# Optimization experiments

Hardware: AMD Instinct MI355X
Metric: run time of the kernel (lower is better)

## Reference

```python
import jax, jax.numpy as jnp
import numpy as np

B, T, D, H = 4, 2048, 1024, 16
DH = D // H
SCALE = 1.0 / np.sqrt(DH)


def setup_inputs() -> dict:
    key = jax.random.key(0)
    ks = jax.random.split(key, 8)
    s = 1.0 / np.sqrt(D)  # keep projections well-scaled
    return {
        "query": jax.random.normal(ks[0], (B, T, D), jnp.float32),
        "key": jax.random.normal(ks[1], (B, T, D), jnp.float32),
        "value": jax.random.normal(ks[2], (B, T, D), jnp.float32),
        "Wq": jax.random.normal(ks[3], (D, D), jnp.float32) * s,
        "bq": jnp.zeros((D,), jnp.float32),
        "Wk": jax.random.normal(ks[4], (D, D), jnp.float32) * s,
        "bk": jnp.zeros((D,), jnp.float32),
        "Wv": jax.random.normal(ks[5], (D, D), jnp.float32) * s,
        "bv": jnp.zeros((D,), jnp.float32),
        "Wo": jax.random.normal(ks[6], (D, D), jnp.float32) * s,
        "bo": jnp.zeros((D,), jnp.float32),
    }


def reference(query, key, value, Wq, bq, Wk, bk, Wv, bv, Wo, bo):
    # Linear projections (torch Linear: x @ W.T + b; W here stored as [out,in])
    Q = query @ Wq.T + bq            # [B,T,D]
    K = key @ Wk.T + bk
    V = value @ Wv.T + bv
    # split heads -> [B,H,T,DH]
    Q = Q.reshape(B, T, H, DH).transpose(0, 2, 1, 3)
    K = K.reshape(B, T, H, DH).transpose(0, 2, 1, 3)
    V = V.reshape(B, T, H, DH).transpose(0, 2, 1, 3)
    # scaled dot-product attention (chunking in the original is a memory
    # optimization, not a math change; no mask, eval-mode dropout = identity)
    scores = jnp.einsum("bhqd,bhkd->bhqk", Q, K) * SCALE
    attn = jax.nn.softmax(scores, axis=-1)
    out = jnp.einsum("bhqk,bhkd->bhqd", attn, V)  # [B,H,T,DH]
    out = out.transpose(0, 2, 1, 3).reshape(B, T, D)
    return out @ Wo.T + bo
```

## Files before the change

### kernel.cpp

```cpp
#include <hip/hip_runtime.h>
#include <hip/hip_bf16.h>

typedef __bf16 bf16x8 __attribute__((ext_vector_type(8)));
typedef float f32x4 __attribute__((ext_vector_type(4)));
typedef float f32x16 __attribute__((ext_vector_type(16)));
typedef unsigned int uint;
typedef unsigned short u16;

#define DEV static __device__ __forceinline__

DEV u16 f2bf(float x) {
    uint u = __builtin_bit_cast(uint, x);
    u += 0x7FFFu + ((u >> 16) & 1u);
    return (u16)(u >> 16);
}

DEV uint cvtpk(float lo, float hi) {
    uint r;
    asm("v_cvt_pk_bf16_f32 %0, %1, %2" : "=v"(r) : "v"(lo), "v"(hi));
    return r;
}

DEV void plswap(uint& a, uint& b) {
    asm("v_permlane32_swap_b32 %0, %1" : "+v"(a), "+v"(b));
}

DEV float max3f(float a, float b, float c) {
    float d;
    asm("v_max3_f32 %0, %1, %2, %3" : "=v"(d) : "v"(a), "v"(b), "v"(c));
    return d;
}

DEV float fexp2(float x) { return __builtin_amdgcn_exp2f(x); }

DEV void gload16(const void* g, void* l) {
    __builtin_amdgcn_global_load_lds((const __attribute__((address_space(1))) void*)g,
                                     (__attribute__((address_space(3))) void*)l,
                                     16, 0, 0);
}

DEV uint4 xpose8(uint4 vd, int l) {
    uint w0 = vd.x, w1 = vd.y, w2 = vd.z, w3 = vd.w;
    {
        int lam = (l >> 5) & 1;
        uint s0 = lam ? w0 : w2, s1 = lam ? w1 : w3;
        uint t0 = __shfl_xor(s0, 32), t1 = __shfl_xor(s1, 32);
        if (lam) { w0 = t0; w1 = t1; } else { w2 = t0; w3 = t1; }
    }
    {
        int lam = (l >> 4) & 1;
        uint s0 = lam ? w0 : w1, s1 = lam ? w2 : w3;
        uint t0 = __shfl_xor(s0, 16), t1 = __shfl_xor(s1, 16);
        if (lam) { w0 = t0; w2 = t1; } else { w1 = t0; w3 = t1; }
    }
    {
        int lam = (l >> 3) & 1;
        uint sA = lam ? ((w0 & 0xFFFFu) | (w1 << 16)) : ((w0 >> 16) | (w1 & 0xFFFF0000u));
        uint sB = lam ? ((w2 & 0xFFFFu) | (w3 << 16)) : ((w2 >> 16) | (w3 & 0xFFFF0000u));
        uint tA = __shfl_xor(sA, 8), tB = __shfl_xor(sB, 8);
        if (lam) {
            w0 = (w0 & 0xFFFF0000u) | (tA & 0xFFFFu);
            w1 = (w1 & 0xFFFF0000u) | (tA >> 16);
            w2 = (w2 & 0xFFFF0000u) | (tB & 0xFFFFu);
            w3 = (w3 & 0xFFFF0000u) | (tB >> 16);
        } else {
            w0 = (w0 & 0xFFFFu) | (tA << 16);
            w1 = (w1 & 0xFFFFu) | (tA & 0xFFFF0000u);
            w2 = (w2 & 0xFFFFu) | (tB << 16);
            w3 = (w3 & 0xFFFFu) | (tB & 0xFFFF0000u);
        }
    }
    return make_uint4(w0, w1, w2, w3);
}

__global__ __launch_bounds__(256) void k_wconv(const float* __restrict__ w0,
                                               const float* __restrict__ w1,
                                               const float* __restrict__ w2,
                                               const float* __restrict__ w3,
                                               u16* __restrict__ out) {
    const int which = blockIdx.x >> 9;
    const float* in = which == 0 ? w0 : (which == 1 ? w1 : (which == 2 ? w2 : w3));
    const long i = (blockIdx.x & 511) * 256 + threadIdx.x;
    const float4* p = (const float4*)in + i * 2;
    float4 a = p[0], b = p[1];
    uint4 dv;
    dv.x = cvtpk(a.x, a.y); dv.y = cvtpk(a.z, a.w);
    dv.z = cvtpk(b.x, b.y); dv.w = cvtpk(b.z, b.w);
    ((uint4*)(out + ((long)which << 20)))[i] = dv;
}

__global__ __launch_bounds__(256, 2) void k_gemm_qkv(
    const float* __restrict__ Aq, const float* __restrict__ Ak,
    const float* __restrict__ Av, const u16* __restrict__ Bw,
    const float* __restrict__ b0, const float* __restrict__ b1,
    const float* __restrict__ b2, u16* __restrict__ Cb) {
    constexpr int N = 1024, K = 1024;
    __shared__ u16 lA[128 * 64];
    __shared__ u16 lB[128 * 64];
    const int tid = threadIdx.x;
    const int l = tid & 63, w = tid >> 6;
    const int lr = l & 15, lk = l >> 4;
    const int wr = w >> 1, wc = w & 1;
    const int nbn = N >> 7;
    const int cpx = (int)gridDim.x >> 3;
    const int wg = (blockIdx.x & 7) * cpx + (blockIdx.x >> 3);
    const int bm = wg / nbn, bn = wg % nbn;
    const int seg = bm >> 6;
    const float* Aseg = seg == 0 ? Aq : (seg == 1 ? Ak : Av);
    const u16* Bseg = Bw + ((long)seg << 20);
    const float* bias = seg == 0 ? b0 : (seg == 1 ? b1 : b2);
    const int bml = bm & 63;

    const int arow = tid >> 3;
    const int acol = (tid & 7) * 8;
    int adst[4];
    const float* asrc[4];
#pragma unroll
    for (int t = 0; t < 4; ++t) {
        int row = t * 32 + arow;
        adst[t] = row * 128 + ((acol * 2) ^ ((row & 7) << 4));
        asrc[t] = Aseg + (long)(bml * 128 + row) * K + acol;
    }
    long bbase[4];
    int bdst[4];
#pragma unroll
    for (int t = 0; t < 4; ++t) {
        int p = (t * 256 + tid) * 16;
        int row = p >> 7;
        int src = (p & 127) ^ ((row & 7) << 4);
        bdst[t] = p;
        bbase[t] = (long)(bn * 128 + row) * (K * 2) + src;
    }
    const int swz = (lr & 7) << 4;
    int aoff[4][2], boff[4][2];
#pragma unroll
    for (int m = 0; m < 4; ++m)
#pragma unroll
        for (int kc = 0; kc < 2; ++kc) {
            aoff[m][kc] = (wr * 64 + m * 16 + lr) * 128 + ((kc * 64 + lk * 16) ^ swz);
            boff[m][kc] = (wc * 64 + m * 16 + lr) * 128 + ((kc * 64 + lk * 16) ^ swz);
        }

    f32x4 acc[4][4] = {};
    const char* gB = (const char*)Bseg;
    const char* lAb = (const char*)lA;
    const char* lBb = (const char*)lB;
    for (int kt = 0; kt < K / 64; ++kt) {
        __syncthreads();
#pragma unroll
        for (int t = 0; t < 4; ++t)
            gload16(gB + bbase[t] + kt * 128, (char*)lB + bdst[t]);
        float4 f0[4], f1[4];
#pragma unroll
        for (int t = 0; t < 4; ++t) {
            const float* s = asrc[t] + kt * 64;
            f0[t] = *(const float4*)s;
            f1[t] = *(const float4*)(s + 4);
        }
#pragma unroll
        for (int t = 0; t < 4; ++t) {
            uint4 dv;
            dv.x = cvtpk(f0[t].x, f0[t].y);
            dv.y = cvtpk(f0[t].z, f0[t].w);
            dv.z = cvtpk(f1[t].x, f1[t].y);
            dv.w = cvtpk(f1[t].z, f1[t].w);
            *(uint4*)((char*)lA + adst[t]) = dv;
        }
        __syncthreads();
#pragma unroll
        for (int kc = 0; kc < 2; ++kc) {
            bf16x8 av[4], bv[4];
#pragma unroll
            for (int m = 0; m < 4; ++m) av[m] = *(const bf16x8*)(lAb + aoff[m][kc]);
#pragma unroll
            for (int n = 0; n < 4; ++n) bv[n] = *(const bf16x8*)(lBb + boff[n][kc]);
#pragma unroll
            for (int m = 0; m < 4; ++m)
#pragma unroll
                for (int n = 0; n < 4; ++n)
                    acc[m][n] = __builtin_amdgcn_mfma_f32_16x16x32_bf16(av[m], bv[n], acc[m][n], 0, 0, 0);
        }
    }

    const int col0 = bn * 128 + wc * 64;
    float bval[4];
#pragma unroll
    for (int n = 0; n < 4; ++n) bval[n] = bias[col0 + n * 16 + lr];
    const int row0 = bm * 128 + wr * 64;
#pragma unroll
    for (int m = 0; m < 4; ++m)
#pragma unroll
        for (int j = 0; j < 4; ++j) {
            int row = row0 + m * 16 + lk * 4 + j;
#pragma unroll
            for (int n = 0; n < 4; ++n)
                Cb[(long)row * N + col0 + n * 16 + lr] = f2bf(acc[m][n][j] + bval[n]);
        }
}

__global__ __launch_bounds__(256) void k_vtrans(const u16* __restrict__ V,
                                                u16* __restrict__ VT) {
    __shared__ u16 lds[64 * 40];
    const int tid = threadIdx.x;
    const int l = tid & 63, w = tid >> 6;
    const int vr = l >> 3, vdb = l & 7;
    const int bid = blockIdx.x;
    const int bh = bid & 63, tc = bid >> 6;
    const int b = bh >> 4, h = bh & 15;
    const int t0 = tc * 32;

    const u16* src = V + ((long)(b * 2048 + t0 + w * 8 + vr) * 1024 + h * 64 + vdb * 8);
    uint4 vd = *(const uint4*)src;
    uint4 tt = xpose8(vd, l);
    *(uint4*)((char*)lds + (vdb * 8 + vr) * 80 + w * 16) = tt;
    __syncthreads();
    const int ch2 = tid >> 2, part = tid & 3;
    uint4 r = *(const uint4*)((const char*)lds + ch2 * 80 + part * 16);
    *(uint4*)(VT + ((long)(bh * 64 + ch2) * 2048 + t0 + part * 8)) = r;
}

__global__ __launch_bounds__(256, 2) void k_gemm_bt(
    const u16* __restrict__ A, const u16* __restrict__ Bw,
    const float* __restrict__ bias, float* __restrict__ Cf,
    int M, int N, int K) {
    __shared__ u16 lA[128 * 64];
    __shared__ u16 lB[128 * 64];
    const int tid = threadIdx.x;
    const int l = tid & 63, w = tid >> 6;
    const int lr = l & 15, lk = l >> 4;
    const int wr = w >> 1, wc = w & 1;
    const int nbn = N >> 7;
    const int cpx = (int)gridDim.x >> 3;
    const int wg = (blockIdx.x & 7) * cpx + (blockIdx.x >> 3);
    const int bm = wg / nbn, bn = wg % nbn;

    long abase[4], bbase[4];
    int ldst[4];
#pragma unroll
    for (int t = 0; t < 4; ++t) {
        int c = t * 256 + tid;
        int p = c * 16;
        int row = p >> 7;
        int inrow = p & 127;
        int src = inrow ^ ((row & 7) << 4);
        ldst[t] = p;
        abase[t] = (long)(bm * 128 + row) * (K * 2) + src;
        bbase[t] = (long)(bn * 128 + row) * (K * 2) + src;
    }
    const int swz = (lr & 7) << 4;
    int aoff[4][2], boff[4][2];
#pragma unroll
    for (int m = 0; m < 4; ++m)
#pragma unroll
        for (int kc = 0; kc < 2; ++kc) {
            aoff[m][kc] = (wr * 64 + m * 16 + lr) * 128 + ((kc * 64 + lk * 16) ^ swz);
            boff[m][kc] = (wc * 64 + m * 16 + lr) * 128 + ((kc * 64 + lk * 16) ^ swz);
        }

    f32x4 acc[4][4] = {};
    const char* gA = (const char*)A;
    const char* gB = (const char*)Bw;
    const char* lAb = (const char*)lA;
    const char* lBb = (const char*)lB;
    const int nkt = K >> 6;
    for (int kt = 0; kt < nkt; ++kt) {
        __syncthreads();
#pragma unroll
        for (int t = 0; t < 4; ++t)
            gload16(gA + abase[t] + kt * 128, (char*)lA + ldst[t]);
#pragma unroll
        for (int t = 0; t < 4; ++t)
            gload16(gB + bbase[t] + kt * 128, (char*)lB + ldst[t]);
        __syncthreads();
#pragma unroll
        for (int kc = 0; kc < 2; ++kc) {
            bf16x8 av[4], bv[4];
#pragma unroll
            for (int m = 0; m < 4; ++m) av[m] = *(const bf16x8*)(lAb + aoff[m][kc]);
#pragma unroll
            for (int n = 0; n < 4; ++n) bv[n] = *(const bf16x8*)(lBb + boff[n][kc]);
#pragma unroll
            for (int m = 0; m < 4; ++m)
#pragma unroll
                for (int n = 0; n < 4; ++n)
                    acc[m][n] = __builtin_amdgcn_mfma_f32_16x16x32_bf16(av[m], bv[n], acc[m][n], 0, 0, 0);
        }
    }

    const int row0 = bm * 128 + wr * 64;
    const int col0 = bn * 128 + wc * 64;
    float bval[4];
#pragma unroll
    for (int n = 0; n < 4; ++n) bval[n] = bias[col0 + n * 16 + lr];
#pragma unroll
    for (int m = 0; m < 4; ++m)
#pragma unroll
        for (int j = 0; j < 4; ++j) {
            int row = row0 + m * 16 + lk * 4 + j;
#pragma unroll
            for (int n = 0; n < 4; ++n)
                Cf[(long)row * N + col0 + n * 16 + lr] = acc[m][n][j] + bval[n];
        }
}

__global__ __launch_bounds__(512, 4) void k_attn5(
    const u16* __restrict__ Qb, const u16* __restrict__ Kb,
    const u16* __restrict__ VTb, u16* __restrict__ Ob) {
    constexpr int T = 2048, D = 1024;
    constexpr int NT = T / 64;
    __shared__ u16 sK[2][4096];
    __shared__ u16 sV[2][4096];
    const int tid = threadIdx.x;
    const int l = tid & 63, w = tid >> 6;
    const int hi = l >> 5;
    const int q32 = l & 31;
    const int hi16 = hi * 16;
    const int kswz = (q32 & 7) << 4;
    const int bid = blockIdx.x;
    const int bh = (bid & 7) * 8 + ((bid >> 3) & 7);
    const int qt = bid >> 6;
    const int b = bh >> 4, h = bh & 15;

    const char* Qg = (const char*)(Qb + (long)b * T * D + h * 64);
    const char* Kg = (const char*)(Kb + (long)b * T * D + h * 64);
    const char* VTg = (const char*)(VTb + (long)bh * 64 * 2048);
    const int q0 = qt * 256 + w * 32;

    bf16x8 qf[4];
#pragma unroll
    for (int c = 0; c < 4; ++c)
        qf[c] = *(const bf16x8*)(Qg + (long)(q0 + q32) * 2048 + c * 32 + hi16);

    const int srow = tid >> 3;
    const int ssrc = ((tid & 7) * 16) ^ ((srow & 7) << 4);
    const int sdst = tid * 16;
    const long kbase = (long)srow * 2048 + ssrc;
    const long vbase = (long)srow * 4096 + ssrc;

    union { u16 s[8]; bf16x8 v; } ones_u;
#pragma unroll
    for (int i = 0; i < 8; ++i) ones_u.s[i] = 0x3F80;
    const bf16x8 onesv = ones_u.v;

#define STAGE(kt_, buf_) do {                                                  \
        gload16(Kg + (long)(kt_) * 64 * 2048 + kbase, (char*)sK[buf_] + sdst); \
        gload16(VTg + (kt_) * 128 + vbase, (char*)sV[buf_] + sdst);            \
    } while (0)

    STAGE(0, 0);
    __syncthreads();

    f32x16 o[2] = {};
    f32x16 lacc = {};
    float m = -1e30f;
    const float k1 = 0.18033688f;
    const float THR = 44.3616f;

    for (int kt = 0; kt < NT; ++kt) {
        if (kt + 1 < NT) STAGE(kt + 1, (kt + 1) & 1);

        const char* kbp = (const char*)sK[kt & 1];
        f32x16 st[2] = {};
        __builtin_amdgcn_s_setprio(1);
#pragma unroll
        for (int c = 0; c < 4; ++c) {
            bf16x8 kf = *(const bf16x8*)(kbp + q32 * 128 + ((c * 32 + hi16) ^ kswz));
            st[0] = __builtin_amdgcn_mfma_f32_32x32x16_bf16(kf, qf[c], st[0], 0, 0, 0);
        }
#pragma unroll
        for (int c = 0; c < 4; ++c) {
            bf16x8 kf = *(const bf16x8*)(kbp + (32 + q32) * 128 + ((c * 32 + hi16) ^ kswz));
            st[1] = __builtin_amdgcn_mfma_f32_32x32x16_bf16(kf, qf[c], st[1], 0, 0, 0);
        }
        __builtin_amdgcn_s_setprio(0);

        float t0 = max3f(st[0][0], st[0][1], st[0][2]);
        float t1 = max3f(st[0][3], st[0][4], st[0][5]);
        float t2 = max3f(st[0][6], st[0][7], st[0][8]);
        float t3 = max3f(st[0][9], st[0][10], st[0][11]);
        float t4 = max3f(st[0][12], st[0][13], st[0][14]);
        float t5 = max3f(st[1][0], st[1][1], st[1][2]);
        float t6 = max3f(st[1][3], st[1][4], st[1][5]);
        float t7 = max3f(st[1][6], st[1][7], st[1][8]);
        float t8 = max3f(st[1][9], st[1][10], st[1][11]);
        float t9 = max3f(st[1][12], st[1][13], st[1][14]);
        float u0 = max3f(t0, t1, t2);
        float u1 = max3f(t3, t4, st[0][15]);
        float u2 = max3f(t5, t6, t7);
        float u3 = max3f(t8, t9, st[1][15]);
        float rm = fmaxf(max3f(u0, u1, u2), u3);

        bool defer = __all(rm <= m + THR);
        if (!defer) {
            float rmw = fmaxf(rm, __shfl_xor(rm, 32));
            float mn = fmaxf(m, rmw);
            float aq = fexp2((m - mn) * k1);
            m = mn;
#pragma unroll
            for (int r = 0; r < 16; ++r) {
                int src = (r & 3) + 8 * (r >> 2) + 4 * hi;
                float ar = __shfl(aq, src);
                o[0][r] *= ar;
                o[1][r] *= ar;
                lacc[r] *= ar;
            }
        }
        float mk = m * k1;
#pragma unroll
        for (int n = 0; n < 2; ++n)
#pragma unroll
            for (int r = 0; r < 16; ++r)
                st[n][r] = fexp2(fmaf(st[n][r], k1, -mk));

        const char* vbp = (const char*)sV[kt & 1];
        __builtin_amdgcn_s_setprio(1);
#pragma unroll
        for (int c = 0; c < 4; ++c) {
            const int n = c >> 1, rb = (c & 1) * 8;
            uint A0 = cvtpk(st[n][rb + 0], st[n][rb + 1]);
            uint A1 = cvtpk(st[n][rb + 2], st[n][rb + 3]);
            uint B0 = cvtpk(st[n][rb + 4], st[n][rb + 5]);
            uint B1 = cvtpk(st[n][rb + 6], st[n][rb + 7]);
            plswap(A0, B0);
            plswap(A1, B1);
            union { uint u[4]; bf16x8 v; } pa;
            pa.u[0] = A0; pa.u[1] = A1; pa.u[2] = B0; pa.u[3] = B1;
            int cb = c * 32 + hi16;
            bf16x8 v0 = *(const bf16x8*)(vbp + q32 * 128 + (cb ^ kswz));
            bf16x8 v1 = *(const bf16x8*)(vbp + (32 + q32) * 128 + (cb ^ kswz));
            o[0] = __builtin_amdgcn_mfma_f32_32x32x16_bf16(pa.v, v0, o[0], 0, 0, 0);
            o[1] = __builtin_amdgcn_mfma_f32_32x32x16_bf16(pa.v, v1, o[1], 0, 0, 0);
            lacc  = __builtin_amdgcn_mfma_f32_32x32x16_bf16(pa.v, onesv, lacc, 0, 0, 0);
        }
        __builtin_amdgcn_s_setprio(0);
        __syncthreads();
    }
#undef STAGE

#pragma unroll
    for (int r = 0; r < 16; ++r) {
        float inv = 1.f / lacc[r];
        int srcq = (r & 3) + 8 * (r >> 2) + 4 * hi;
        int trow = q0 + srcq;
        char* orow = (char*)Ob + ((long)(b * T + trow) * D + h * 64) * 2;
        *(u16*)(orow + q32 * 2) = f2bf(o[0][r] * inv);
        *(u16*)(orow + (32 + q32) * 2) = f2bf(o[1][r] * inv);
    }
}

extern "C" void kernel_launch(void* const* d_in, const int* in_sizes, int n_in,
                              void* d_out, int out_size, void* d_ws, size_t ws_size,
                              hipStream_t stream) {
    const float* q  = (const float*)d_in[0];
    const float* k  = (const float*)d_in[1];
    const float* v  = (const float*)d_in[2];
    const float* Wq = (const float*)d_in[3];
    const float* bq = (const float*)d_in[4];
    const float* Wk = (const float*)d_in[5];
    const float* bk = (const float*)d_in[6];
    const float* Wv = (const float*)d_in[7];
    const float* bv = (const float*)d_in[8];
    const float* Wo = (const float*)d_in[9];
    const float* bo = (const float*)d_in[10];

    const long MT = 8192L * 1024;
    const long WT = 1024L * 1024;
    u16* ws   = (u16*)d_ws;
    u16* wall = ws;
    u16* qbf  = wall + 4 * WT;
    u16* kbf  = qbf + MT;
    u16* vbf  = kbf + MT;
    u16* vtb  = vbf + MT;
    u16* abf  = vtb + MT;

    k_wconv<<<dim3(2048), dim3(256), 0, stream>>>(Wq, Wk, Wv, Wo, wall);

    k_gemm_qkv<<<dim3(1536), dim3(256), 0, stream>>>(q, k, v, wall,
                                                     bq, bk, bv, qbf);

    k_vtrans<<<dim3(4096), dim3(256), 0, stream>>>(vbf, vtb);

    k_attn5<<<dim3(512), dim3(512), 0, stream>>>(qbf, kbf, vtb, abf);

    k_gemm_bt<<<dim3(512), dim3(256), 0, stream>>>(abf, wall + 3 * WT, bo,
                                                   (float*)d_out, 8192, 1024, 1024);
}
```

Baseline: 192.9 us.

## Double-buffer LDS tiles in QKV GEMM to overlap global loads with MFMA

New measurement: 201.8 us. +4.6%, slower.

```diff
diff --git a/kernel.cpp b/kernel.cpp
--- a/kernel.cpp
+++ b/kernel.cpp
@@ -95,8 +95,8 @@
     const float* __restrict__ b0, const float* __restrict__ b1,
     const float* __restrict__ b2, u16* __restrict__ Cb) {
     constexpr int N = 1024, K = 1024;
-    __shared__ u16 lA[128 * 64];
-    __shared__ u16 lB[128 * 64];
+    __shared__ u16 lA[2][8192];
+    __shared__ u16 lB[2][8192];
     const int tid = threadIdx.x;
     const int l = tid & 63, w = tid >> 6;
     const int lr = l & 15, lk = l >> 4;
@@ -143,30 +143,46 @@
 
     f32x4 acc[4][4] = {};
     const char* gB = (const char*)Bseg;
-    const char* lAb = (const char*)lA;
-    const char* lBb = (const char*)lB;
+    float4 f0[4], f1[4];
+
+#define LOADA(kt_) do {                                                        \
+        _Pragma("unroll")                                                      \
+        for (int t = 0; t < 4; ++t) {                                          \
+            const float* s = asrc[t] + (kt_) * 64;                             \
+            f0[t] = *(const float4*)s;                                         \
+            f1[t] = *(const float4*)(s + 4);                                   \
+        }                                                                      \
+    } while (0)
+#define WRITEA(buf_) do {                                                      \
+        _Pragma("unroll")                                                      \
+        for (int t = 0; t < 4; ++t) {                                          \
+            uint4 dv;                                                          \
+            dv.x = cvtpk(f0[t].x, f0[t].y);                                    \
+            dv.y = cvtpk(f0[t].z, f0[t].w);                                    \
+            dv.z = cvtpk(f1[t].x, f1[t].y);                                    \
+            dv.w = cvtpk(f1[t].z, f1[t].w);                                    \
+            *(uint4*)((char*)lA[buf_] + adst[t]) = dv;                         \
+        }                                                                      \
+    } while (0)
+#define LOADB(kt_, buf_) do {                                                  \
+        _Pragma("unroll")                                                      \
+        for (int t = 0; t < 4; ++t)                                            \
+            gload16(gB + bbase[t] + (kt_) * 128, (char*)lB[buf_] + bdst[t]);   \
+    } while (0)
+
+    LOADA(0);
+    LOADB(0, 0);
+    WRITEA(0);
+    __syncthreads();
+
     for (int kt = 0; kt < K / 64; ++kt) {
-        __syncthreads();
-#pragma unroll
-        for (int t = 0; t < 4; ++t)
-            gload16(gB + bbase[t] + kt * 128, (char*)lB + bdst[t]);
-        float4 f0[4], f1[4];
-#pragma unroll
-        for (int t = 0; t < 4; ++t) {
-            const float* s = asrc[t] + kt * 64;
-            f0[t] = *(const float4*)s;
-            f1[t] = *(const float4*)(s + 4);
-        }
-#pragma unroll
-        for (int t = 0; t < 4; ++t) {
-            uint4 dv;
-            dv.x = cvtpk(f0[t].x, f0[t].y);
-            dv.y = cvtpk(f0[t].z, f0[t].w);
-            dv.z = cvtpk(f1[t].x, f1[t].y);
-            dv.w = cvtpk(f1[t].z, f1[t].w);
-            *(uint4*)((char*)lA + adst[t]) = dv;
-        }
-        __syncthreads();
+        const int cur = kt & 1;
+        if (kt + 1 < K / 64) {
+            LOADB(kt + 1, cur ^ 1);
+            LOADA(kt + 1);
+        }
+        const char* lAb = (const char*)lA[cur];
+        const char* lBb = (const char*)lB[cur];
 #pragma unroll
         for (int kc = 0; kc < 2; ++kc) {
             bf16x8 av[4], bv[4];
@@ -180,7 +196,13 @@
                 for (int n = 0; n < 4; ++n)
                     acc[m][n] = __builtin_amdgcn_mfma_f32_16x16x32_bf16(av[m], bv[n], acc[m][n], 0, 0, 0);
         }
-    }
+        if (kt + 1 < K / 64)
+            WRITEA(cur ^ 1);
+        __syncthreads();
+    }
+#undef LOADA
+#undef WRITEA
+#undef LOADB
 
     const int col0 = bn * 128 + wc * 64;
     float bval[4];
```

## Pre-convert QKV activations to bf16 and load them with async LDS copies

Applied to the files above, without the earlier changes.

New measurement: 208.2 us. 8.0% more time.

```diff
diff --git a/kernel.cpp b/kernel.cpp
--- a/kernel.cpp
+++ b/kernel.cpp
@@ -89,9 +89,23 @@
     ((uint4*)(out + ((long)which << 20)))[i] = dv;
 }
 
+__global__ __launch_bounds__(256) void k_aconv(const float* __restrict__ q,
+                                               const float* __restrict__ k,
+                                               const float* __restrict__ v,
+                                               u16* __restrict__ out) {
+    const int which = blockIdx.x >> 12;
+    const float* in = which == 0 ? q : (which == 1 ? k : v);
+    const long i = (long)(blockIdx.x & 4095) * 256 + threadIdx.x;
+    const float4* p = (const float4*)in + i * 2;
+    float4 a = p[0], b = p[1];
+    uint4 dv;
+    dv.x = cvtpk(a.x, a.y); dv.y = cvtpk(a.z, a.w);
+    dv.z = cvtpk(b.x, b.y); dv.w = cvtpk(b.z, b.w);
+    ((uint4*)(out + ((long)which << 23)))[i] = dv;
+}
+
 __global__ __launch_bounds__(256, 2) void k_gemm_qkv(
-    const float* __restrict__ Aq, const float* __restrict__ Ak,
-    const float* __restrict__ Av, const u16* __restrict__ Bw,
+    const u16* __restrict__ A, const u16* __restrict__ Bw,
     const float* __restrict__ b0, const float* __restrict__ b1,
     const float* __restrict__ b2, u16* __restrict__ Cb) {
     constexpr int N = 1024, K = 1024;
@@ -106,29 +120,20 @@
     const int wg = (blockIdx.x & 7) * cpx + (blockIdx.x >> 3);
     const int bm = wg / nbn, bn = wg % nbn;
     const int seg = bm >> 6;
-    const float* Aseg = seg == 0 ? Aq : (seg == 1 ? Ak : Av);
     const u16* Bseg = Bw + ((long)seg << 20);
     const float* bias = seg == 0 ? b0 : (seg == 1 ? b1 : b2);
-    const int bml = bm & 63;
-
-    const int arow = tid >> 3;
-    const int acol = (tid & 7) * 8;
-    int adst[4];
-    const float* asrc[4];
+
+    long abase[4], bbase[4];
+    int ldst[4];
 #pragma unroll
     for (int t = 0; t < 4; ++t) {
-        int row = t * 32 + arow;
-        adst[t] = row * 128 + ((acol * 2) ^ ((row & 7) << 4));
-        asrc[t] = Aseg + (long)(bml * 128 + row) * K + acol;
-    }
-    long bbase[4];
-    int bdst[4];
-#pragma unroll
-    for (int t = 0; t < 4; ++t) {
-        int p = (t * 256 + tid) * 16;
+        int c = t * 256 + tid;
+        int p = c * 16;
         int row = p >> 7;
-        int src = (p & 127) ^ ((row & 7) << 4);
-        bdst[t] = p;
+        int inrow = p & 127;
+        int src = inrow ^ ((row & 7) << 4);
+        ldst[t] = p;
+        abase[t] = (long)(bm * 128 + row) * (K * 2) + src;
         bbase[t] = (long)(bn * 128 + row) * (K * 2) + src;
     }
     const int swz = (lr & 7) << 4;
@@ -142,6 +147,7 @@
         }
 
     f32x4 acc[4][4] = {};
+    const char* gA = (const char*)A;
     const char* gB = (const char*)Bseg;
     const char* lAb = (const char*)lA;
     const char* lBb = (const char*)lB;
@@ -149,23 +155,10 @@
         __syncthreads();
 #pragma unroll
         for (int t = 0; t < 4; ++t)
-            gload16(gB + bbase[t] + kt * 128, (char*)lB + bdst[t]);
-        float4 f0[4], f1[4];
-#pragma unroll
-        for (int t = 0; t < 4; ++t) {
-            const float* s = asrc[t] + kt * 64;
-            f0[t] = *(const float4*)s;
-            f1[t] = *(const float4*)(s + 4);
-        }
-#pragma unroll
-        for (int t = 0; t < 4; ++t) {
-            uint4 dv;
-            dv.x = cvtpk(f0[t].x, f0[t].y);
-            dv.y = cvtpk(f0[t].z, f0[t].w);
-            dv.z = cvtpk(f1[t].x, f1[t].y);
-            dv.w = cvtpk(f1[t].z, f1[t].w);
-            *(uint4*)((char*)lA + adst[t]) = dv;
-        }
+            gload16(gA + abase[t] + kt * 128, (char*)lA + ldst[t]);
+#pragma unroll
+        for (int t = 0; t < 4; ++t)
+            gload16(gB + bbase[t] + kt * 128, (char*)lB + ldst[t]);
         __syncthreads();
 #pragma unroll
         for (int kc = 0; kc < 2; ++kc) {
@@ -467,15 +460,17 @@
     const long WT = 1024L * 1024;
     u16* ws   = (u16*)d_ws;
     u16* wall = ws;
-    u16* qbf  = wall + 4 * WT;
+    u16* xall = wall + 4 * WT;
+    u16* qbf  = xall + 3 * MT;
     u16* kbf  = qbf + MT;
     u16* vbf  = kbf + MT;
     u16* vtb  = vbf + MT;
-    u16* abf  = vtb + MT;
+    u16* abf  = xall;
 
     k_wconv<<<dim3(2048), dim3(256), 0, stream>>>(Wq, Wk, Wv, Wo, wall);
-
-    k_gemm_qkv<<<dim3(1536), dim3(256), 0, stream>>>(q, k, v, wall,
+    k_aconv<<<dim3(12288), dim3(256), 0, stream>>>(q, k, v, xall);
+
+    k_gemm_qkv<<<dim3(1536), dim3(256), 0, stream>>>(xall, wall,
                                                      bq, bk, bv, qbf);
 
     k_vtrans<<<dim3(4096), dim3(256), 0, stream>>>(vbf, vtb);
```
